# Kernel optimization log

Hardware: AMD Instinct MI355X
Metric: run time of the kernel (lower is better)

Reference implementation:

```python
import jax, jax.numpy as jnp
import numpy as np
from jax import lax

NPOINTS = [1024, 256, 64, 16]
RADII = [0.02, 0.04, 0.06, 0.08]
NSAMPLE = [32, 32, 16, 16]
# per-level MLP widths; first entry already includes the +3 for use_xyz concat
MLPS = [[6, 32, 32, 64], [67, 64, 64, 128], [131, 128, 128, 256], [259, 256, 256, 512]]
EPS = 1e-5


def setup_inputs() -> dict:
    key = jax.random.key(0)
    B, N = 8, 16384
    pc = jax.random.uniform(jax.random.fold_in(key, 0), (B, N, 6), jnp.float32)
    # xyz into a 0.2-cube so the hard-coded radii (0.02..0.08) find real neighborhoods
    pc = pc.at[..., :3].multiply(0.2)
    inp = {"pointcloud": pc}
    ki = 1
    for l, m in enumerate(MLPS):
        for j in range(len(m) - 1):
            cin, cout = m[j], m[j + 1]
            inp[f"w{l}{j}"] = jax.random.normal(jax.random.fold_in(key, ki), (cin, cout), jnp.float32) * (1.0 / float(np.sqrt(cin)))
            inp[f"g{l}{j}"] = jnp.ones((cout,), jnp.float32)
            inp[f"b{l}{j}"] = jnp.zeros((cout,), jnp.float32)
            ki += 1
    return inp


def _fps(xyz, npoint):
    # iterative farthest point sampling, start at index 0 (matches CUDA kernel)
    B, N, _ = xyz.shape

    def step(carry, _):
        mind, last = carry
        lastp = jnp.take_along_axis(xyz, last[:, None, None], axis=1)  # [B,1,3]
        d = jnp.sum((xyz - lastp) ** 2, axis=-1)                       # [B,N]
        mind = jnp.minimum(mind, d)
        nxt = jnp.argmax(mind, axis=1).astype(jnp.int32)
        return (mind, nxt), last

    init = (jnp.full((B, N), 1e10, xyz.dtype), jnp.zeros((B,), jnp.int32))
    _, idx = lax.scan(step, init, None, length=npoint)
    return jnp.transpose(idx)  # [B,npoint]


def _gather(pts, idx):
    # pts [B,N,C], idx [B,...] -> [B,...,C]
    return jax.vmap(lambda p, i: p[i])(pts, idx)


def _ball_query(xyz, centers, radius, nsample):
    # first nsample points (in index order) within radius; pad with first hit (0 if none)
    N = xyz.shape[1]
    d2 = jnp.sum((centers[:, :, None, :] - xyz[:, None, :, :]) ** 2, axis=-1)  # [B,S,N]
    key = jnp.where(d2 < radius * radius, jnp.arange(N, dtype=jnp.int32), N)
    negtop, _ = lax.top_k(-key, nsample)
    sel = -negtop                      # ascending candidate indices
    valid = sel < N
    first = jnp.where(valid[..., :1], sel[..., :1], 0)
    return jnp.where(valid, sel, first)  # [B,S,nsample] int32


def _sa(xyz, feats, npoint, radius, nsample, layers):
    fps_idx = lax.stop_gradient(_fps(xyz, npoint))
    new_xyz = _gather(xyz, fps_idx)                    # [B,S,3]
    idx = _ball_query(xyz, new_xyz, radius, nsample)   # [B,S,K]
    g = _gather(xyz, idx) - new_xyz[:, :, None, :]     # centered grouped xyz [B,S,K,3]
    g = jnp.concatenate([g, _gather(feats, idx)], axis=-1)  # use_xyz concat -> [B,S,K,3+C]
    x = g
    for W, gamma, beta in layers:
        x = jnp.einsum('bski,io->bsko', x, W)          # 1x1 conv, bias=False (bn on)
        mu = jnp.mean(x, axis=(0, 1, 2))               # BN training-mode batch stats
        var = jnp.var(x, axis=(0, 1, 2))
        x = jax.nn.relu(gamma * (x - mu) * lax.rsqrt(var + EPS) + beta)
    return new_xyz, jnp.max(x, axis=2)                 # max-pool over neighbors -> [B,S,Cout]


def reference(pointcloud, w00, g00, b00, w01, g01, b01, w02, g02, b02,
              w10, g10, b10, w11, g11, b11, w12, g12, b12,
              w20, g20, b20, w21, g21, b21, w22, g22, b22,
              w30, g30, b30, w31, g31, b31, w32, g32, b32):
    params = [
        [(w00, g00, b00), (w01, g01, b01), (w02, g02, b02)],
        [(w10, g10, b10), (w11, g11, b11), (w12, g12, b12)],
        [(w20, g20, b20), (w21, g21, b21), (w22, g22, b22)],
        [(w30, g30, b30), (w31, g31, b31), (w32, g32, b32)],
    ]
    xyz = pointcloud[..., :3]
    feats = pointcloud[..., 3:]   # channels-last (torch keeps [B,C,N]; pure layout diff)
    l_xyz, l_feats = [xyz], [feats]
    for k in range(4):
        nx, nf = _sa(l_xyz[k], l_feats[k], NPOINTS[k], RADII[k], NSAMPLE[k], params[k])
        l_xyz.append(nx)
        l_feats.append(nf)
    return tuple(l_xyz) + tuple(l_feats)
```

## Files before the change

kernel.cpp:

```cpp
#include <hip/hip_runtime.h>

#define WAVE 64

__global__ __launch_bounds__(256) void split_kernel(const float* __restrict__ pc,
    float* __restrict__ xyz, float* __restrict__ feats, int total) {
  int t = blockIdx.x * blockDim.x + threadIdx.x;
  if (t >= total) return;
  const float* p = pc + (size_t)t * 6;
  xyz[t * 3 + 0] = p[0]; xyz[t * 3 + 1] = p[1]; xyz[t * 3 + 2] = p[2];
  feats[t * 3 + 0] = p[3]; feats[t * 3 + 1] = p[4]; feats[t * 3 + 2] = p[5];
}

__global__ __launch_bounds__(256) void zero_kernel(float* __restrict__ p, int n) {
  int t = blockIdx.x * blockDim.x + threadIdx.x;
  if (t < n) p[t] = 0.f;
}

__device__ __forceinline__ unsigned long long dpp_max_u64(unsigned long long v) {
#define DPP_STEP_U64(ctrl) { \
    unsigned lo_ = (unsigned)v, hi_ = (unsigned)(v >> 32); \
    unsigned tlo_ = (unsigned)__builtin_amdgcn_update_dpp((int)lo_, (int)lo_, ctrl, 0xf, 0xf, false); \
    unsigned thi_ = (unsigned)__builtin_amdgcn_update_dpp((int)hi_, (int)hi_, ctrl, 0xf, 0xf, false); \
    unsigned long long t_ = ((unsigned long long)thi_ << 32) | tlo_; \
    if (t_ > v) v = t_; }
  DPP_STEP_U64(0x111) DPP_STEP_U64(0x112) DPP_STEP_U64(0x114)
  DPP_STEP_U64(0x118) DPP_STEP_U64(0x142) DPP_STEP_U64(0x143)
#undef DPP_STEP_U64
  return v;
}

#define FPS_W   8
#define FPS_PT  8
__global__ __launch_bounds__(256, 4) void fps_big_multi_kernel(
    const float* __restrict__ xyz, float* __restrict__ new_xyz,
    unsigned long long* __restrict__ gkey, int N, int S) {
  const int b = blockIdx.x & 7;
  const int w = blockIdx.x >> 3;
  const int tid = threadIdx.x;
  const int lane = tid & 63;
  const int wv = tid >> 6;
  const float* px = xyz + (size_t)b * N * 3;
  const int base = w * (FPS_PT * 256);
  __shared__ unsigned long long s_cand[4];
  __shared__ unsigned long long s_win;
  float rx[FPS_PT], ry[FPS_PT], rz[FPS_PT], mind[FPS_PT];
#pragma unroll
  for (int p = 0; p < FPS_PT; ++p) {
    int i = base + p * 256 + tid;
    rx[p] = px[i * 3 + 0]; ry[p] = px[i * 3 + 1]; rz[p] = px[i * 3 + 2];
    asm volatile("" : "+v"(rx[p]), "+v"(ry[p]), "+v"(rz[p]));
    mind[p] = 1e10f;
  }
  float qx = px[0], qy = px[1], qz = px[2];
  if (w == 0 && tid == 0) {
    float* o = new_xyz + (size_t)b * S * 3;
    o[0] = qx; o[1] = qy; o[2] = qz;
  }
  unsigned long long* slots = gkey + (size_t)b * S * FPS_W;
  for (unsigned it = 1; it < (unsigned)S; ++it) {
    float bestv = -1.f; unsigned besti = 0;
#pragma unroll
    for (int p = 0; p < FPS_PT; ++p) {
      float dx = __fsub_rn(rx[p], qx);
      float dy = __fsub_rn(ry[p], qy);
      float dz = __fsub_rn(rz[p], qz);
      float d = __fadd_rn(__fadd_rn(__fmul_rn(dx, dx), __fmul_rn(dy, dy)), __fmul_rn(dz, dz));
      float mo = fminf(mind[p], d);
      mind[p] = mo;
      if (mo > bestv) { bestv = mo; besti = (unsigned)(base + p * 256 + tid); }
    }
    unsigned long long key = ((unsigned long long)__float_as_uint(bestv) << 32)
                           | (0xFFFFFFFFu - besti);
    key = dpp_max_u64(key);
    if (lane == 63) s_cand[wv] = key;
    __syncthreads();
    if (tid < 64) {
      unsigned long long k = s_cand[lane & 3];
#pragma unroll
      for (int off = 1; off < 4; off <<= 1) {
        unsigned long long o = __shfl_xor(k, off, 4);
        if (o > k) k = o;
      }
      if (lane == 0) {
        atomicExch(&slots[(size_t)it * FPS_W + w], k);
      }
      unsigned long long kk = 0ull;
      if (lane < FPS_W) {
        unsigned long long* sl = &slots[(size_t)it * FPS_W + lane];
        unsigned long long t0 = __builtin_amdgcn_s_memrealtime();
        int r = 0;
        for (;;) {
          kk = __hip_atomic_load(sl, __ATOMIC_RELAXED, __HIP_MEMORY_SCOPE_AGENT);
          if (kk) break;
          if (++r > 256) {
            kk = atomicMax(sl, 0ull);
            if (kk) break;
            if (__builtin_amdgcn_s_memrealtime() - t0 > 2000000ull) {
              kk = 0xFFFFFFFFull;
              break;
            }
            __builtin_amdgcn_s_sleep(1);
          }
        }
      }
#pragma unroll
      for (int off = 1; off < FPS_W; off <<= 1) {
        unsigned long long o = __shfl_xor(kk, off, FPS_W);
        if (o > kk) kk = o;
      }
      if (lane == 0) s_win = kk;
    }
    __syncthreads();
    unsigned long long k = s_win;
    int last = (int)((0xFFFFFFFFu - (unsigned)k) & 16383u);
    const float* q = px + (size_t)last * 3;
    qx = q[0]; qy = q[1]; qz = q[2];
    if (w == 0 && tid == 0) {
      float* o = new_xyz + ((size_t)b * S + it) * 3;
      o[0] = qx; o[1] = qy; o[2] = qz;
    }
  }
}

__global__ void fps_small_kernel(const float* __restrict__ xyz,
    float* __restrict__ new_xyz, int N, int S) {
  const int b = blockIdx.x;
  const int tid = threadIdx.x;
  const int lane = tid & 63;
  const float* px = xyz + (size_t)b * N * 3;
  __shared__ float sx[1024], sy[1024], sz[1024];
  __shared__ unsigned long long s_key[3];
  float x = px[tid * 3 + 0], y = px[tid * 3 + 1], z = px[tid * 3 + 2];
  sx[tid] = x; sy[tid] = y; sz[tid] = z;
  if (tid < 3) s_key[tid] = 0ull;
  float mind = 1e10f;
  float qx = px[0], qy = px[1], qz = px[2];
  if (tid == 0) {
    float* o = new_xyz + (size_t)b * S * 3;
    o[0] = qx; o[1] = qy; o[2] = qz;
  }
  __syncthreads();
  for (unsigned it = 1; it < (unsigned)S; ++it) {
    float dx = __fsub_rn(x, qx);
    float dy = __fsub_rn(y, qy);
    float dz = __fsub_rn(z, qz);
    float d = __fadd_rn(__fadd_rn(__fmul_rn(dx, dx), __fmul_rn(dy, dy)), __fmul_rn(dz, dz));
    mind = fminf(mind, d);
    unsigned long long key = ((unsigned long long)__float_as_uint(mind) << 32)
                           | (0xFFFFFFFFu - (unsigned)tid);
    key = dpp_max_u64(key);
    if (lane == 63) atomicMax(&s_key[it % 3u], key);
    if (tid == 0) s_key[(it + 1) % 3u] = 0ull;
    __syncthreads();
    unsigned long long k = s_key[it % 3u];
    int last = (int)(0xFFFFFFFFu - (unsigned)k);
    qx = sx[last]; qy = sy[last]; qz = sz[last];
    if (tid == 0) {
      float* o = new_xyz + ((size_t)b * S + it) * 3;
      o[0] = qx; o[1] = qy; o[2] = qz;
    }
  }
}

__global__ __launch_bounds__(256) void ballquery_kernel(const float* __restrict__ xyz,
    const float* __restrict__ centers, int* __restrict__ out_idx,
    int N, int S, int nsample, float r2) {
  int gw = (blockIdx.x * blockDim.x + threadIdx.x) >> 6;
  int lane = threadIdx.x & 63;
  int b = gw / S;
  int s = gw - b * S;
  const float* px = xyz + (size_t)b * N * 3;
  const float* cp = centers + ((size_t)b * S + s) * 3;
  float cx = cp[0], cy = cp[1], cz = cp[2];
  int* out = out_idx + ((size_t)b * S + s) * nsample;
  int cnt = 0;
  int firsti = 0;
  for (int base = 0; base < N; base += WAVE) {
    int i = base + lane;
    float dx = __fsub_rn(cx, px[i * 3 + 0]);
    float dy = __fsub_rn(cy, px[i * 3 + 1]);
    float dz = __fsub_rn(cz, px[i * 3 + 2]);
    float d = __fadd_rn(__fadd_rn(__fmul_rn(dx, dx), __fmul_rn(dy, dy)), __fmul_rn(dz, dz));
    bool hit = d < r2;
    unsigned long long m = __ballot(hit);
    if (hit) {
      int slot = cnt + __popcll(m & ((1ull << lane) - 1ull));
      if (slot < nsample) out[slot] = i;
    }
    if (cnt == 0 && m) firsti = base + __ffsll((unsigned long long)m) - 1;
    cnt += __popcll(m);
    if (cnt >= nsample) break;
  }
  for (int q = cnt + lane; q < nsample; q += WAVE) out[q] = firsti;
}

__global__ __launch_bounds__(256) void group_kernel(const float* __restrict__ xyz,
    const float* __restrict__ feats, const float* __restrict__ centers,
    const int* __restrict__ idx, float* __restrict__ X,
    int N, int S, int K, int ci, int R) {
  int t = blockIdx.x * blockDim.x + threadIdx.x;
  int C0 = ci + 3;
  int r = t / C0;
  if (r >= R) return;
  int c = t - r * C0;
  int g = r / K;
  int b = g / S;
  int j = idx[r];
  float v;
  if (c < 3) v = __fsub_rn(xyz[((size_t)b * N + j) * 3 + c], centers[(size_t)g * 3 + c]);
  else       v = feats[((size_t)b * N + j) * ci + (c - 3)];
  X[(size_t)r * C0 + c] = v;
}

#define BM 64
#define BN 64
#define BK 16
__global__ __launch_bounds__(256) void mm_fused_kernel(const float* __restrict__ A,
    const float* __restrict__ W, float* __restrict__ Y,
    float* __restrict__ st_out, const float* __restrict__ st_in,
    const float* __restrict__ g_in, const float* __restrict__ b_in,
    int R, int C, int Co, float inv_n) {
  __shared__ float As[BK][BM + 4];
  __shared__ float Bs[BK][BN + 4];
  __shared__ float s_mu[260], s_rs[260], s_g[260], s_b[260];
  __shared__ float s_sum[BN], s_sq[BN];
  int r0 = blockIdx.x * BM;
  int n0 = blockIdx.y * BN;
  int tid = threadIdx.x;
  int tx = tid & 15, ty = tid >> 4;
  if (st_in) {
    for (int c = tid; c < C; c += 256) {
      float mu = st_in[c] * inv_n;
      float var = st_in[512 + c] * inv_n - mu * mu;
      s_mu[c] = mu; s_rs[c] = rsqrtf(var + 1e-5f);
      s_g[c] = g_in[c]; s_b[c] = b_in[c];
    }
  }
  if (tid < BN) { s_sum[tid] = 0.f; s_sq[tid] = 0.f; }
  __syncthreads();
  float acc[4][4] = {};
  for (int k0 = 0; k0 < C; k0 += BK) {
#pragma unroll
    for (int u = 0; u < 4; ++u) {
      int lin = tid + u * 256;
      int row = lin >> 4;
      int cc = lin & 15;
      int c = k0 + cc;
      float v = 0.f;
      if (c < C) {
        v = A[(size_t)(r0 + row) * C + c];
        if (st_in) {
          v = s_g[c] * ((v - s_mu[c]) * s_rs[c]) + s_b[c];
          v = v > 0.f ? v : 0.f;
        }
      }
      As[cc][row] = v;
    }
#pragma unroll
    for (int u = 0; u < 4; ++u) {
      int lin = tid + u * 256;
      int kk = lin >> 6;
      int n = lin & 63;
      int c = k0 + kk;
      Bs[kk][n] = (c < C && (n0 + n) < Co) ? W[(size_t)c * Co + n0 + n] : 0.f;
    }
    __syncthreads();
#pragma unroll
    for (int kk = 0; kk < BK; ++kk) {
      float a0[4], b0[4];
#pragma unroll
      for (int i = 0; i < 4; ++i) a0[i] = As[kk][ty * 4 + i];
#pragma unroll
      for (int jj = 0; jj < 4; ++jj) b0[jj] = Bs[kk][tx * 4 + jj];
#pragma unroll
      for (int i = 0; i < 4; ++i)
#pragma unroll
        for (int jj = 0; jj < 4; ++jj)
          acc[i][jj] = fmaf(a0[i], b0[jj], acc[i][jj]);
    }
    __syncthreads();
  }
#pragma unroll
  for (int i = 0; i < 4; ++i) {
    int r = r0 + ty * 4 + i;
#pragma unroll
    for (int jj = 0; jj < 4; ++jj) {
      int n = n0 + tx * 4 + jj;
      if (n < Co) Y[(size_t)r * Co + n] = acc[i][jj];
    }
  }
#pragma unroll
  for (int jj = 0; jj < 4; ++jj) {
    float cs = 0.f, cq = 0.f;
#pragma unroll
    for (int i = 0; i < 4; ++i) { float v = acc[i][jj]; cs += v; cq += v * v; }
    atomicAdd(&s_sum[tx * 4 + jj], cs);
    atomicAdd(&s_sq[tx * 4 + jj], cq);
  }
  __syncthreads();
  if (tid < BN) {
    int n = n0 + tid;
    if (n < Co) {
      atomicAdd(&st_out[n], s_sum[tid]);
      atomicAdd(&st_out[512 + n], s_sq[tid]);
    }
  }
}

__global__ __launch_bounds__(256) void norm_relu_max_kernel(const float* __restrict__ Y,
    float* __restrict__ O, const float* __restrict__ st,
    const float* __restrict__ gamma, const float* __restrict__ beta,
    int G, int K, int Co, float inv_n) {
  int t = blockIdx.x * blockDim.x + threadIdx.x;
  if (t >= G * Co) return;
  int c = t & (Co - 1);
  int g = t / Co;
  float mu = st[c] * inv_n;
  float var = st[512 + c] * inv_n - mu * mu;
  float rs = rsqrtf(var + 1e-5f);
  float ga = gamma[c], be = beta[c];
  const float* yp = Y + (size_t)g * K * Co + c;
  float m = -1e30f;
  for (int k = 0; k < K; ++k) {
    float v = ga * ((yp[(size_t)k * Co] - mu) * rs) + be;
    m = fmaxf(m, v);
  }
  O[t] = m > 0.f ? m : 0.f;
}

extern "C" void kernel_launch(void* const* d_in, const int* in_sizes, int n_in,
                              void* d_out, int out_size, void* d_ws, size_t ws_size,
                              hipStream_t stream) {
  const float* pc = (const float*)d_in[0];
  float* out = (float*)d_out;
  char* wsb = (char*)d_ws;

  int* ballidx = (int*)wsb;
  float* stats = (float*)(wsb + ((size_t)1 << 20));
  unsigned long long* gkey = (unsigned long long*)(wsb + ((size_t)2 << 20));
  float* bufA = (float*)(wsb + ((size_t)3 << 20));
  float* bufB = (float*)(wsb + ((size_t)37 << 20));

  const int B = 8;
  static const int Ns[4] = {16384, 1024, 256, 64};
  static const int Ss[4] = {1024, 256, 64, 16};
  static const int Ks[4] = {32, 32, 16, 16};
  static const double Rr[4] = {0.02, 0.04, 0.06, 0.08};
  static const int Ci[4] = {3, 64, 128, 256};
  static const int mlp[4][4] = {{6,32,32,64},{67,64,64,128},{131,128,128,256},{259,256,256,512}};
  static const size_t ox[5] = {0, 393216, 417792, 423936, 425472};
  static const size_t of[5] = {425856, 819072, 1343360, 1605504, 1736576};

  split_kernel<<<(B * 16384 + 255) / 256, 256, 0, stream>>>(pc, out + ox[0], out + of[0], B * 16384);
  zero_kernel<<<(524288 + 255) / 256, 256, 0, stream>>>(stats, 524288);

  for (int l = 0; l < 4; ++l) {
    const float* xyz = out + ox[l];
    const float* fts = out + of[l];
    float* nxyz = out + ox[l + 1];
    const int N = Ns[l], S = Ss[l], K = Ks[l], ci = Ci[l], C0 = ci + 3;
    const float r2 = (float)(Rr[l] * Rr[l]);

    if (l == 0) fps_big_multi_kernel<<<B * FPS_W, 256, 0, stream>>>(xyz, nxyz, gkey, N, S);
    else        fps_small_kernel<<<B, N, 0, stream>>>(xyz, nxyz, N, S);

    ballquery_kernel<<<(B * S) / 4, 256, 0, stream>>>(xyz, nxyz, ballidx, N, S, K, r2);

    const int R = B * S * K;
    {
      int total = R * C0;
      group_kernel<<<(total + 255) / 256, 256, 0, stream>>>(xyz, fts, nxyz, ballidx, bufA,
                                                            N, S, K, ci, R);
    }

    const float inv_n = 1.0f / (float)R;
    float* X = bufA; float* Y = bufB;
    const float* prev_st = nullptr;
    const float* prev_g = nullptr;
    const float* prev_b = nullptr;
    for (int j = 0; j < 3; ++j) {
      const int cin = mlp[l][j], cout = mlp[l][j + 1];
      const float* Wt = (const float*)d_in[1 + (l * 3 + j) * 3 + 0];
      const float* Ga = (const float*)d_in[1 + (l * 3 + j) * 3 + 1];
      const float* Be = (const float*)d_in[1 + (l * 3 + j) * 3 + 2];
      float* st = stats + (size_t)(l * 3 + j) * 1024;
      dim3 grid(R / 64, (cout + 63) / 64);
      mm_fused_kernel<<<grid, 256, 0, stream>>>(X, Wt, Y, st, prev_st, prev_g, prev_b,
                                                R, cin, cout, inv_n);
      if (j < 2) {
        prev_st = st; prev_g = Ga; prev_b = Be;
        float* tswap = X; X = Y; Y = tswap;
      } else {
        int G = B * S;
        int tot = G * cout;
        norm_relu_max_kernel<<<(tot + 255) / 256, 256, 0, stream>>>(Y, out + of[l + 1], st, Ga, Be,
                                                                    G, K, cout, inv_n);
      }
    }
  }
}
```

Baseline: 2.382 ms.

## Let every wave poll cross-block FPS slots, dropping the broadcast barrier

In the multi-block farthest-point-sampling kernel, each wave now spin-polls the global per-iteration slots itself and reduces the winner with DPP plus readlane. Previously wave 0 polled and broadcast the result through shared memory behind a second __syncthreads. The change removes one block barrier and a shared-memory round trip per iteration. The poll loop issues two loads per pass, drops the s_sleep back-off and retries the atomic fallback less often. A one-time read over the batch's point cloud is added to warm the cache for the later winner-coordinate loads, at the cost of more global polling traffic from all waves.

```diff
diff --git a/kernel.cpp b/kernel.cpp
--- a/kernel.cpp
+++ b/kernel.cpp
@@ -42,7 +42,6 @@
   const float* px = xyz + (size_t)b * N * 3;
   const int base = w * (FPS_PT * 256);
   __shared__ unsigned long long s_cand[4];
-  __shared__ unsigned long long s_win;
   float rx[FPS_PT], ry[FPS_PT], rz[FPS_PT], mind[FPS_PT];
 #pragma unroll
   for (int p = 0; p < FPS_PT; ++p) {
@@ -50,6 +49,16 @@
     rx[p] = px[i * 3 + 0]; ry[p] = px[i * 3 + 1]; rz[p] = px[i * 3 + 2];
     asm volatile("" : "+v"(rx[p]), "+v"(ry[p]), "+v"(rz[p]));
     mind[p] = 1e10f;
+  }
+  {
+    const float4* p4 = reinterpret_cast<const float4*>(px);
+    float s0 = 0.f;
+    const int n4 = N * 3 / 4;
+    for (int i = tid; i < n4; i += 256) {
+      float4 v = p4[i];
+      s0 += v.x + v.y + v.z + v.w;
+    }
+    asm volatile("" :: "v"(s0));
   }
   float qx = px[0], qy = px[1], qz = px[2];
   if (w == 0 && tid == 0) {
@@ -74,45 +83,40 @@
     key = dpp_max_u64(key);
     if (lane == 63) s_cand[wv] = key;
     __syncthreads();
-    if (tid < 64) {
-      unsigned long long k = s_cand[lane & 3];
+    if (wv == 0) {
+      unsigned long long kw = s_cand[lane & 3];
 #pragma unroll
       for (int off = 1; off < 4; off <<= 1) {
-        unsigned long long o = __shfl_xor(k, off, 4);
-        if (o > k) k = o;
+        unsigned long long o = __shfl_xor(kw, off, 4);
+        if (o > kw) kw = o;
       }
       if (lane == 0) {
-        atomicExch(&slots[(size_t)it * FPS_W + w], k);
+        atomicExch(&slots[(size_t)it * FPS_W + w], kw);
       }
-      unsigned long long kk = 0ull;
-      if (lane < FPS_W) {
-        unsigned long long* sl = &slots[(size_t)it * FPS_W + lane];
-        unsigned long long t0 = __builtin_amdgcn_s_memrealtime();
-        int r = 0;
-        for (;;) {
-          kk = __hip_atomic_load(sl, __ATOMIC_RELAXED, __HIP_MEMORY_SCOPE_AGENT);
-          if (kk) break;
-          if (++r > 256) {
-            kk = atomicMax(sl, 0ull);
-            if (kk) break;
-            if (__builtin_amdgcn_s_memrealtime() - t0 > 2000000ull) {
-              kk = 0xFFFFFFFFull;
-              break;
-            }
-            __builtin_amdgcn_s_sleep(1);
+    }
+    unsigned long long k = 0ull;
+    if (lane < FPS_W) {
+      unsigned long long* sl = &slots[(size_t)it * FPS_W + lane];
+      unsigned long long t0 = __builtin_amdgcn_s_memrealtime();
+      int r = 0;
+      for (;;) {
+        unsigned long long k1 = __hip_atomic_load(sl, __ATOMIC_RELAXED, __HIP_MEMORY_SCOPE_AGENT);
+        unsigned long long k2 = __hip_atomic_load(sl, __ATOMIC_RELAXED, __HIP_MEMORY_SCOPE_AGENT);
+        if (k1) { k = k1; break; }
+        if (k2) { k = k2; break; }
+        if ((++r & 31) == 0) {
+          k = atomicMax(sl, 0ull);
+          if (k) break;
+          if (__builtin_amdgcn_s_memrealtime() - t0 > 2000000ull) {
+            k = 0xFFFFFFFFull;
+            break;
           }
         }
       }
-#pragma unroll
-      for (int off = 1; off < FPS_W; off <<= 1) {
-        unsigned long long o = __shfl_xor(kk, off, FPS_W);
-        if (o > kk) kk = o;
-      }
-      if (lane == 0) s_win = kk;
-    }
-    __syncthreads();
-    unsigned long long k = s_win;
-    int last = (int)((0xFFFFFFFFu - (unsigned)k) & 16383u);
+    }
+    k = dpp_max_u64(k);
+    unsigned klo = (unsigned)__builtin_amdgcn_readlane((int)(unsigned)k, 63);
+    int last = (int)((0xFFFFFFFFu - klo) & 16383u);
     const float* q = px + (size_t)last * 3;
     qx = q[0]; qy = q[1]; qz = q[2];
     if (w == 0 && tid == 0) {
```

New measurement: 2.583 ms. 1.08x slower.
